# Kernel tuning notes

Measured on AMD Instinct MI355X. Metric: run time of the kernel, lower is better.

Reference implementation:

```python
import jax, jax.numpy as jnp
import numpy as np

DIM = 2048
ORDER = 4
L_MAX = 2048
BATCH = 4  # must equal ORDER due to broadcast in the original module
SEQ = 2048


def setup_inputs() -> dict:
    key = jax.random.key(0)
    k1, k2 = jax.random.split(key)
    x = jax.random.normal(k1, (BATCH, DIM, SEQ), dtype=jnp.float32)
    kernel = jax.random.normal(k2, (ORDER, DIM, L_MAX), dtype=jnp.float32) * 0.02
    bias = jnp.zeros((DIM,), dtype=jnp.float32)
    return {"x": x, "kernel": kernel, "bias": bias}


def reference(x, kernel, bias):
    # x: (B, dim, L); kernel: (order, dim, l_max); B == order by broadcast
    seq_len = x.shape[-1]
    n = 2 * seq_len  # zero-padded FFT length for linear (causal) convolution
    x_fft = jnp.fft.rfft(x, n=n, axis=-1)            # (B, dim, n//2+1) complex
    kernel_fft = jnp.fft.rfft(kernel, n=n, axis=-1)  # (order, dim, n//2+1)
    y_fft = x_fft * kernel_fft                       # broadcast: B == order
    y = jnp.fft.irfft(y_fft, n=n, axis=-1)[:, :, :seq_len]
    return y + x + bias[None, :, None]
```

## Files before the change

kernel.cpp:

```cpp
#include <hip/hip_runtime.h>

typedef __attribute__((ext_vector_type(8)))  short short8;
typedef __attribute__((ext_vector_type(16))) float f32x16;
typedef unsigned int uint;
typedef unsigned long long ull;

#define SEQ    2048
#define XPITCH 20
#define XSZ    (64 * XPITCH)
#define KSZ    1040
#define WSZ    (XSZ + KSZ)
#define LDSU   (4 * WSZ + 16)

__device__ inline uint pack_bf16_2(float lo, float hi) {
    uint ul = __float_as_uint(lo);
    uint uh = __float_as_uint(hi);
    ul = (ul + 0x7fffu + ((ul >> 16) & 1u)) >> 16;
    uh = (uh + 0x7fffu + ((uh >> 16) & 1u)) >> 16;
    return (ul & 0xffffu) | (uh << 16);
}

#define MFMA(A, B, C) __builtin_amdgcn_mfma_f32_32x32x16_bf16( \
    __builtin_bit_cast(short8, A), __builtin_bit_cast(short8, B), C, 0, 0, 0)

__device__ inline uint fnl(uint h, uint l, uint sh) {
    return (uint)((((ull)h << 32) | l) >> sh);
}

#define SEL4(W0, W1, W2, W3, W4, W5, OUT) {                          \
    uint t0 = c2 ? (W1) : (W0), t1 = c2 ? (W2) : (W1),               \
         t2 = c2 ? (W3) : (W2), t3 = c2 ? (W4) : (W3),               \
         t4 = c2 ? (W5) : (W4);                                      \
    OUT.x = fnl(t1, t0, sh); OUT.y = fnl(t2, t1, sh);                \
    OUT.z = fnl(t3, t2, sh); OUT.w = fnl(t4, t3, sh); }

__global__ __launch_bounds__(256, 4)
void hyena_mfma(const float* __restrict__ x, const float* __restrict__ kern,
                const float* __restrict__ bias, float* __restrict__ out)
{
    __shared__ __align__(16) uint lds[LDSU];
    char* ldsb = (char*)lds;

    const int tid = threadIdx.x;
    const int wid = tid >> 6;
    const int l   = tid & 63;
    const int n   = l & 31;
    const int hi  = l >> 5;
    const int row = blockIdx.x * 4 + wid;
    const size_t rb = (size_t)row * SEQ;

    uint* xw = lds + wid * WSZ;
    uint* kw = xw + XSZ;

    #pragma unroll
    for (int it = 0; it < 16; ++it) {
        const int e = it * 128 + 2 * l;
        float2 v = *(const float2*)&x[rb + e];
        xw[(e >> 5) * XPITCH + ((e & 31) >> 1)] = pack_bf16_2(v.x, v.y);
    }
    #pragma unroll
    for (int it = 0; it < 16; ++it) {
        const int j = it * 128 + 2 * l;
        float2 v = *(const float2*)&kern[rb + (2046 - j)];
        kw[j >> 1] = pack_bf16_2(v.y, v.x);
    }
    if (l < 16) kw[1024 + l] = 0u;
    if (tid < 16) lds[4 * WSZ + tid] = 0u;
    __syncthreads();

    const int st00 = 2047 - n + 8 * hi;
    const bool c2  = (st00 & 2) != 0;
    const uint sh  = (uint)(st00 & 1) << 4;
    int vk  = (wid * WSZ + XSZ) * 4 + ((st00 & ~3) << 1) - 2048;
    int va2 = wid * WSZ * 4 + (n + 32) * 80 + 16 * hi;
    const int vz = 4 * WSZ * 4 + 16 * hi;

    f32x16 acc0 = {}, acc1a = {}, acc1b = {};

    #pragma unroll 2
    for (int r = 0; r < 32; ++r) {
        const int va = (n >= r) ? (va2 - 2560) : vz;
        const uint4 a00 = *(const uint4*)(ldsb + va);
        const uint4 a01 = *(const uint4*)(ldsb + va + 32);
        const uint4 a10 = *(const uint4*)(ldsb + va2);
        const uint4 a11 = *(const uint4*)(ldsb + va2 + 32);

        uint2 q0, q1, q2;
        uint4 B;
        q0 = *(const uint2*)(ldsb + vk + 2048);
        q1 = *(const uint2*)(ldsb + vk + 2056);
        q2 = *(const uint2*)(ldsb + vk + 2064);
        SEL4(q0.x, q0.y, q1.x, q1.y, q2.x, q2.y, B);
        acc0  = MFMA(a00, B, acc0);
        acc1a = MFMA(a10, B, acc1a);
        q0 = *(const uint2*)(ldsb + vk + 2080);
        q1 = *(const uint2*)(ldsb + vk + 2088);
        q2 = *(const uint2*)(ldsb + vk + 2096);
        SEL4(q0.x, q0.y, q1.x, q1.y, q2.x, q2.y, B);
        acc0  = MFMA(a01, B, acc0);
        acc1a = MFMA(a11, B, acc1a);
        q0 = *(const uint2*)(ldsb + vk);
        q1 = *(const uint2*)(ldsb + vk + 8);
        q2 = *(const uint2*)(ldsb + vk + 16);
        SEL4(q0.x, q0.y, q1.x, q1.y, q2.x, q2.y, B);
        acc1b = MFMA(a00, B, acc1b);
        q0 = *(const uint2*)(ldsb + vk + 32);
        q1 = *(const uint2*)(ldsb + vk + 40);
        q2 = *(const uint2*)(ldsb + vk + 48);
        SEL4(q0.x, q0.y, q1.x, q1.y, q2.x, q2.y, B);
        acc1b = MFMA(a01, B, acc1b);

        va2 -= 80;
        vk  -= 64;
    }

    const float bv = bias[row & 2047];
    #pragma unroll
    for (int mt = 0; mt < 2; ++mt) {
        #pragma unroll
        for (int t = 0; t < 16; ++t) {
            const int rloc = (t & 3) + 8 * (t >> 2) + 4 * hi;
            const int p = mt * 32 + rloc;
            const uint w = xw[p * XPITCH + (n >> 1)];
            const float xr = __uint_as_float((n & 1) ? (w & 0xffff0000u) : (w << 16));
            const float a = mt ? (acc1a[t] + acc1b[t]) : acc0[t];
            out[rb + (size_t)p * 32 + n] = a + xr + bv;
        }
    }
}

extern "C" void kernel_launch(void* const* d_in, const int* in_sizes, int n_in,
                              void* d_out, int out_size, void* d_ws, size_t ws_size,
                              hipStream_t stream) {
    const float* x    = (const float*)d_in[0];
    const float* kern = (const float*)d_in[1];
    const float* bias = (const float*)d_in[2];
    float* out = (float*)d_out;

    hipLaunchKernelGGL(hyena_mfma, dim3(2048), dim3(256), 0, stream,
                       x, kern, bias, out);
}
```

Baseline: 74.60 us.

## Precompute half-shifted kernel copy in LDS to drop per-lane funnel-shift selects

Adds a second LDS copy of the reversed bf16 kernel, shifted by one element. Each lane can then read its B operands directly with plain dword loads instead of loading six words and doing a conditional select plus funnel shift per operand. The X tile pitch drops from 20 to 17 words, which changes the LDS bank pattern. LDS per block grows, so the launch-bounds occupancy hint goes from 4 to 3 blocks, and an extra barrier and copy pass are added before the main loop. The new unaligned scalar dword reads may be split into more LDS instructions or hit bank conflicts.

```diff
diff --git a/kernel.cpp b/kernel.cpp
--- a/kernel.cpp
+++ b/kernel.cpp
@@ -3,13 +3,12 @@
 typedef __attribute__((ext_vector_type(8)))  short short8;
 typedef __attribute__((ext_vector_type(16))) float f32x16;
 typedef unsigned int uint;
-typedef unsigned long long ull;
 
 #define SEQ    2048
-#define XPITCH 20
+#define XPITCH 17
 #define XSZ    (64 * XPITCH)
 #define KSZ    1040
-#define WSZ    (XSZ + KSZ)
+#define WSZ    (XSZ + 2 * KSZ)
 #define LDSU   (4 * WSZ + 16)
 
 __device__ inline uint pack_bf16_2(float lo, float hi) {
@@ -23,18 +22,7 @@
 #define MFMA(A, B, C) __builtin_amdgcn_mfma_f32_32x32x16_bf16( \
     __builtin_bit_cast(short8, A), __builtin_bit_cast(short8, B), C, 0, 0, 0)
 
-__device__ inline uint fnl(uint h, uint l, uint sh) {
-    return (uint)((((ull)h << 32) | l) >> sh);
-}
-
-#define SEL4(W0, W1, W2, W3, W4, W5, OUT) {                          \
-    uint t0 = c2 ? (W1) : (W0), t1 = c2 ? (W2) : (W1),               \
-         t2 = c2 ? (W3) : (W2), t3 = c2 ? (W4) : (W3),               \
-         t4 = c2 ? (W5) : (W4);                                      \
-    OUT.x = fnl(t1, t0, sh); OUT.y = fnl(t2, t1, sh);                \
-    OUT.z = fnl(t3, t2, sh); OUT.w = fnl(t4, t3, sh); }
-
-__global__ __launch_bounds__(256, 4)
+__global__ __launch_bounds__(256, 3)
 void hyena_mfma(const float* __restrict__ x, const float* __restrict__ kern,
                 const float* __restrict__ bias, float* __restrict__ out)
 {
@@ -48,9 +36,11 @@
     const int hi  = l >> 5;
     const int row = blockIdx.x * 4 + wid;
     const size_t rb = (size_t)row * SEQ;
+    const float bv = bias[row & 2047];
 
     uint* xw = lds + wid * WSZ;
-    uint* kw = xw + XSZ;
+    uint* kA = xw + XSZ;
+    uint* kB = kA + KSZ;
 
     #pragma unroll
     for (int it = 0; it < 16; ++it) {
@@ -62,59 +52,56 @@
     for (int it = 0; it < 16; ++it) {
         const int j = it * 128 + 2 * l;
         float2 v = *(const float2*)&kern[rb + (2046 - j)];
-        kw[j >> 1] = pack_bf16_2(v.y, v.x);
+        kA[j >> 1] = pack_bf16_2(v.y, v.x);
     }
-    if (l < 16) kw[1024 + l] = 0u;
+    if (l < 16) kA[1024 + l] = 0u;
+    __syncthreads();
+
+    #pragma unroll
+    for (int it = 0; it < 17; ++it) {
+        const int m = it * 64 + l;
+        if (m < 1039) kB[m] = (kA[m] >> 16) | (kA[m + 1] << 16);
+    }
+    if (l == 0)   kB[1039] = 0u;
     if (tid < 16) lds[4 * WSZ + tid] = 0u;
     __syncthreads();
 
     const int st00 = 2047 - n + 8 * hi;
-    const bool c2  = (st00 & 2) != 0;
-    const uint sh  = (uint)(st00 & 1) << 4;
-    int vk  = (wid * WSZ + XSZ) * 4 + ((st00 & ~3) << 1) - 2048;
-    int va2 = wid * WSZ * 4 + (n + 32) * 80 + 16 * hi;
+    int vb1 = (wid * WSZ + XSZ + (st00 & 1) * KSZ + (st00 >> 1)) * 4;
+    int vb2 = vb1 - 2048;
+    int va2 = wid * WSZ * 4 + (n + 32) * (XPITCH * 4) + 16 * hi;
     const int vz = 4 * WSZ * 4 + 16 * hi;
 
     f32x16 acc0 = {}, acc1a = {}, acc1b = {};
 
     #pragma unroll 2
     for (int r = 0; r < 32; ++r) {
-        const int va = (n >= r) ? (va2 - 2560) : vz;
+        const int va = (n >= r) ? (va2 - 32 * XPITCH * 4) : vz;
         const uint4 a00 = *(const uint4*)(ldsb + va);
         const uint4 a01 = *(const uint4*)(ldsb + va + 32);
         const uint4 a10 = *(const uint4*)(ldsb + va2);
         const uint4 a11 = *(const uint4*)(ldsb + va2 + 32);
 
-        uint2 q0, q1, q2;
-        uint4 B;
-        q0 = *(const uint2*)(ldsb + vk + 2048);
-        q1 = *(const uint2*)(ldsb + vk + 2056);
-        q2 = *(const uint2*)(ldsb + vk + 2064);
-        SEL4(q0.x, q0.y, q1.x, q1.y, q2.x, q2.y, B);
-        acc0  = MFMA(a00, B, acc0);
-        acc1a = MFMA(a10, B, acc1a);
-        q0 = *(const uint2*)(ldsb + vk + 2080);
-        q1 = *(const uint2*)(ldsb + vk + 2088);
-        q2 = *(const uint2*)(ldsb + vk + 2096);
-        SEL4(q0.x, q0.y, q1.x, q1.y, q2.x, q2.y, B);
-        acc0  = MFMA(a01, B, acc0);
-        acc1a = MFMA(a11, B, acc1a);
-        q0 = *(const uint2*)(ldsb + vk);
-        q1 = *(const uint2*)(ldsb + vk + 8);
-        q2 = *(const uint2*)(ldsb + vk + 16);
-        SEL4(q0.x, q0.y, q1.x, q1.y, q2.x, q2.y, B);
-        acc1b = MFMA(a00, B, acc1b);
-        q0 = *(const uint2*)(ldsb + vk + 32);
-        q1 = *(const uint2*)(ldsb + vk + 40);
-        q2 = *(const uint2*)(ldsb + vk + 48);
-        SEL4(q0.x, q0.y, q1.x, q1.y, q2.x, q2.y, B);
-        acc1b = MFMA(a01, B, acc1b);
+        const uint* k1 = (const uint*)(ldsb + vb1);
+        const uint* k2 = (const uint*)(ldsb + vb2);
+        uint4 b00, b01, b10, b11;
+        b00.x = k1[0]; b00.y = k1[1]; b00.z = k1[2];  b00.w = k1[3];
+        b01.x = k1[8]; b01.y = k1[9]; b01.z = k1[10]; b01.w = k1[11];
+        b10.x = k2[0]; b10.y = k2[1]; b10.z = k2[2];  b10.w = k2[3];
+        b11.x = k2[8]; b11.y = k2[9]; b11.z = k2[10]; b11.w = k2[11];
 
-        va2 -= 80;
-        vk  -= 64;
+        acc0  = MFMA(a00, b00, acc0);
+        acc1a = MFMA(a10, b00, acc1a);
+        acc0  = MFMA(a01, b01, acc0);
+        acc1a = MFMA(a11, b01, acc1a);
+        acc1b = MFMA(a00, b10, acc1b);
+        acc1b = MFMA(a01, b11, acc1b);
+
+        va2 -= XPITCH * 4;
+        vb1 -= 64;
+        vb2 -= 64;
     }
 
-    const float bv = bias[row & 2047];
     #pragma unroll
     for (int mt = 0; mt < 2; ++mt) {
         #pragma unroll
```

Measured after the change: 139.2 us. +86.6%, slower.
